# Kernel optimization log

Hardware: AMD Instinct MI355X
Metric: run time of the kernel (lower is better)

## Reference

```python
import jax, jax.numpy as jnp
import numpy as np

B, T, C = 2, 2048, 1280
H, D = 10, 128  # n_head, head_dim (n_kv_head == n_head, so no repeat)
EPS = 1e-5
NEG = -1e9


def setup_inputs() -> dict:
    key = jax.random.key(0)
    ks = jax.random.split(key, 7)
    s = 0.02
    return {
        "x": jax.random.normal(ks[0], (B, T, C), jnp.float32),
        "cos": jax.random.normal(ks[1], (1, 1, T, D // 2), jnp.float32),
        "sin": jax.random.normal(ks[2], (1, 1, T, D // 2), jnp.float32),
        "Wq": jax.random.normal(ks[3], (C, C), jnp.float32) * s,
        "Wk": jax.random.normal(ks[4], (C, C), jnp.float32) * s,
        "Wv": jax.random.normal(ks[5], (C, C), jnp.float32) * s,
        "Wproj": jax.random.normal(ks[6], (C, C), jnp.float32) * s,
    }


def _rope(x, cos, sin):
    # x: [b,h,t,d]; split last dim in half
    x1, x2 = jnp.split(x, 2, axis=-1)
    y1 = x1 * cos + x2 * sin
    y2 = -x1 * sin + x2 * cos
    return jnp.concatenate([y1, y2], axis=-1)


def _rms_norm(x):
    mean = jnp.mean(x * x, axis=-1, keepdims=True)
    return x / jnp.sqrt(mean + EPS)


def reference(x, cos, sin, Wq, Wk, Wv, Wproj):
    b, t, c = x.shape
    # nn.Linear: y = x @ W.T; weights stored [out, in]
    q = (x @ Wq.T).reshape(b, t, H, D).transpose(0, 2, 1, 3)  # [b,h,t,d]
    k = (x @ Wk.T).reshape(b, t, H, D).transpose(0, 2, 1, 3)
    v = (x @ Wv.T).reshape(b, t, H, D).transpose(0, 2, 1, 3)
    q = _rms_norm(_rope(q, cos, sin))
    k = _rms_norm(_rope(k, cos, sin))
    scale = 1.0 / jnp.sqrt(jnp.float32(D))
    scores = jnp.einsum("bhqd,bhkd->bhqk", q, k) * scale
    mask = jnp.triu(jnp.ones((t, t), scores.dtype), k=1)  # 1 above diagonal
    scores = scores + mask * NEG
    attn = jax.nn.softmax(scores, axis=-1)
    y = jnp.einsum("bhqk,bhkd->bhqd", attn, v)
    y = y.transpose(0, 2, 1, 3).reshape(b, t, c)
    return y @ Wproj.T
```

## Files before the change

kernel.cpp:

```cpp
#include <hip/hip_runtime.h>
#include <hip/hip_bf16.h>

#define B_ 2
#define T_ 2048
#define C_ 1280
#define H_ 10
#define D_ 128
#define BT_ (B_*T_)

typedef __hip_bfloat16 bf16;
typedef __attribute__((ext_vector_type(8))) short short8;
typedef __attribute__((ext_vector_type(4))) float f32x4;

__device__ __forceinline__ float bf2f(bf16 v){ return __bfloat162float(v); }
__device__ __forceinline__ bf16  f2bf(float v){ return __float2bfloat16(v); }
__device__ __forceinline__ void stv(bf16* p, float v){ *p = f2bf(v); }
__device__ __forceinline__ void stv(float* p, float v){ *p = v; }

struct alignas(8) bf4 { bf16 a,b,c,d; };

__device__ __forceinline__ void gl2lds(const bf16* g, bf16* l) {
    __builtin_amdgcn_global_load_lds(
        (const __attribute__((address_space(1))) void*)g,
        (__attribute__((address_space(3))) void*)l,
        16, 0, 0);
}

__global__ __launch_bounds__(256)
void cvt(const float* __restrict__ s, bf16* __restrict__ d)
{
    const int i = (blockIdx.x*256 + threadIdx.x)*4;
    const float4 v = *(const float4*)(s + i);
    bf4 o = { f2bf(v.x), f2bf(v.y), f2bf(v.z), f2bf(v.w) };
    *(bf4*)(d + i) = o;
}

__global__ __launch_bounds__(256)
void cvtW(const float* __restrict__ s0, const float* __restrict__ s1,
          const float* __restrict__ s2, const float* __restrict__ s3,
          bf16* __restrict__ d)
{
    const int w = blockIdx.y;
    const float* s = (w==0)?s0:(w==1)?s1:(w==2)?s2:s3;
    const int i = (blockIdx.x*256 + threadIdx.x)*4;
    const float4 v = *(const float4*)(s + i);
    bf4 o = { f2bf(v.x), f2bf(v.y), f2bf(v.z), f2bf(v.w) };
    *(bf4*)(d + (size_t)w*C_*C_ + i) = o;
}

template <typename OT>
__global__ __launch_bounds__(256,3)
void gemm_nt(const bf16* __restrict__ A, const bf16* __restrict__ Wb,
             OT* __restrict__ O0, OT* __restrict__ O1, OT* __restrict__ O2)
{
    __shared__ __align__(16) bf16 As[128*64];
    __shared__ __align__(16) bf16 Bs[128*64];
    const int z = blockIdx.z;
    const bf16* Wm = Wb + (size_t)z*C_*C_;
    OT*         Om = (z==0) ? O0 : (z==1) ? O1 : O2;
    const int wave = threadIdx.x >> 6;
    const int lane = threadIdx.x & 63;
    const int l15 = lane & 15, quad = lane >> 4;
    const int row0 = blockIdx.x*128;
    const int col0 = blockIdx.y*128;
    const int wm = (wave>>1)*64, wn = (wave&1)*64;
    const int srow = lane >> 3;
    const int scol = (lane & 7)*8;

    const f32x4 fzero = {0.f,0.f,0.f,0.f};
    f32x4 acc[4][4];
    #pragma unroll
    for (int i=0;i<4;i++)
        #pragma unroll
        for (int j=0;j<4;j++) acc[i][j] = fzero;

    const bf16* Ag = A  + (size_t)(row0 + wave*32 + srow)*C_ + scol;
    const bf16* Bg = Wm + (size_t)(col0 + wave*32 + srow)*C_ + scol;
    bf16* Al = As + (wave*32)*64;
    bf16* Bl = Bs + (wave*32)*64;

    for (int k0 = 0; k0 < C_; k0 += 64) {
        __syncthreads();
        #pragma unroll
        for (int i=0;i<4;i++){
            gl2lds(Ag + (size_t)i*8*C_ + k0, Al + i*8*64);
            gl2lds(Bg + (size_t)i*8*C_ + k0, Bl + i*8*64);
        }
        asm volatile("s_waitcnt vmcnt(0)" ::: "memory");
        __syncthreads();
        #pragma unroll
        for (int h=0; h<2; ++h) {
            short8 af[4], bfv[4];
            #pragma unroll
            for (int mt=0; mt<4; ++mt) af[mt]  = *(const short8*)(As + (wm + mt*16 + l15)*64 + h*32 + quad*8);
            #pragma unroll
            for (int nt=0; nt<4; ++nt) bfv[nt] = *(const short8*)(Bs + (wn + nt*16 + l15)*64 + h*32 + quad*8);
            #pragma unroll
            for (int mt=0; mt<4; ++mt)
                #pragma unroll
                for (int nt=0; nt<4; ++nt)
                    acc[mt][nt] = __builtin_amdgcn_mfma_f32_16x16x32_bf16(af[mt], bfv[nt], acc[mt][nt], 0,0,0);
        }
    }
    #pragma unroll
    for (int mt=0; mt<4; ++mt)
        #pragma unroll
        for (int nt=0; nt<4; ++nt)
            #pragma unroll
            for (int r=0; r<4; ++r)
                stv(&Om[(size_t)(row0 + wm + mt*16 + quad*4 + r)*C_ + col0 + wn + nt*16 + l15], acc[mt][nt][r]);
}

__global__ __launch_bounds__(256)
void rope_rms(bf16* __restrict__ q, bf16* __restrict__ k,
              const float* __restrict__ cosp, const float* __restrict__ sinp)
{
    const int wave = threadIdx.x >> 6, lane = threadIdx.x & 63;
    const long rb = (long)blockIdx.x*4 + wave;
    const int h = (int)(rb % H_);
    const long bt = rb / H_;
    const int t = (int)(bt % T_);
    bf16* buf = blockIdx.y ? k : q;
    const size_t base = (size_t)bt*C_ + (size_t)h*D_;
    float x1 = bf2f(buf[base + lane]);
    float x2 = bf2f(buf[base + 64 + lane]);
    float c  = cosp[(size_t)t*64 + lane];
    float s  = sinp[(size_t)t*64 + lane];
    float y1 =  x1*c + x2*s;
    float y2 = -x1*s + x2*c;
    float ss = y1*y1 + y2*y2;
    #pragma unroll
    for (int off=1; off<64; off<<=1) ss += __shfl_xor(ss, off);
    float sc = rsqrtf(ss*(1.0f/128.0f) + 1e-5f);
    buf[base + lane]      = f2bf(y1*sc);
    buf[base + 64 + lane] = f2bf(y2*sc);
}

__global__ __launch_bounds__(256)
void vtrans(const bf16* __restrict__ V, bf16* __restrict__ Vt)
{
    __shared__ float st[64][65];
    const int tid = threadIdx.x;
    const int bh = blockIdx.z;
    const int b = bh / H_, h = bh % H_;
    const int t0 = blockIdx.x*64, d0 = blockIdx.y*64;
    #pragma unroll
    for (int i=0;i<16;i++){
        int e = tid + i*256;
        int r = e >> 6, dd = e & 63;
        st[r][dd] = bf2f(V[(size_t)(b*T_ + t0 + r)*C_ + h*D_ + d0 + dd]);
    }
    __syncthreads();
    #pragma unroll
    for (int i=0;i<16;i++){
        int e = tid + i*256;
        int dd = e >> 6, r = e & 63;
        Vt[((size_t)bh*D_ + d0 + dd)*T_ + t0 + r] = f2bf(st[r][dd]);
    }
}

#define M0_ 11.3137085f
__global__ __launch_bounds__(256,3)
void attn(const bf16* __restrict__ Q, const bf16* __restrict__ K,
          const bf16* __restrict__ Vt, bf16* __restrict__ Y,
          bf16* __restrict__ opart, float* __restrict__ lpart)
{
    __shared__ __align__(16) bf16 kbuf[64*128];
    __shared__ __align__(16) bf16 vbuf[128*64];
    __shared__ __align__(16) bf16 ptile[4][16*72];
    const int wave = threadIdx.x >> 6, lane = threadIdx.x & 63;
    const int l15 = lane & 15, quad = lane >> 4;
    const int bid = blockIdx.x;
    const int bh = bid/48, u = bid%48;
    const bool split = (u < 32);
    const int t  = split ? (31 - (u>>1)) : (47 - u);
    const int s  = split ? (u & 1) : 0;
    const int b = bh / H_, h = bh % H_;
    const int t0 = t*64;
    const int nch = t + 1;
    const int cbeg = split ? (s*nch)>>1 : 0;
    const int cend = split ? ((s+1)*nch)>>1 : nch;
    const size_t base = (size_t)b*T_*C_ + (size_t)h*D_;
    const bf16* Kbh = K + base;
    const bf16* Vbh = Vt + (size_t)bh*D_*T_;
    const int t0w = t0 + wave*16;
    const float scale = 0.08838834764831845f;
    bf16* pt = ptile[wave];

    short8 qa[4];
    {
        const bf16* qp = Q + base + (size_t)(t0w + l15)*C_ + quad*8;
        #pragma unroll
        for (int kb4=0; kb4<4; ++kb4) qa[kb4] = *(const short8*)(qp + kb4*32);
    }
    const f32x4 fzero = {0.f,0.f,0.f,0.f};
    f32x4 o[8];
    #pragma unroll
    for (int dt=0; dt<8; ++dt) o[dt] = fzero;
    float lp[4] = {0.f,0.f,0.f,0.f};

    const int vr_off = lane >> 3;
    const int vu     = lane & 7;

    for (int ch=cbeg; ch<cend; ++ch) {
        const int k0 = ch*64;
        __syncthreads();
        #pragma unroll
        for (int j=0;j<4;j++){
            const int row = wave*16 + j*4 + quad;
            const int ug  = (l15 - row) & 15;
            gl2lds(Kbh + (size_t)(k0 + row)*C_ + ug*8, &kbuf[(wave*16 + j*4)*128]);
        }
        #pragma unroll
        for (int j=0;j<4;j++){
            const int r  = wave*32 + j*8 + vr_off;
            const int ug = (vu - r) & 7;
            gl2lds(Vbh + (size_t)r*T_ + k0 + ug*8, &vbuf[(wave*32 + j*8)*64]);
        }
        asm volatile("s_waitcnt vmcnt(0)" ::: "memory");
        __syncthreads();

        f32x4 sc4[4];
        #pragma unroll
        for (int c=0;c<4;c++) sc4[c] = fzero;
        #pragma unroll
        for (int c=0;c<4;c++){
            short8 kf[4];
            #pragma unroll
            for (int kb4=0; kb4<4; ++kb4) {
                const int up = (kb4*4 + quad + l15) & 15;
                kf[kb4] = *(const short8*)(&kbuf[(c*16 + l15)*128 + up*8]);
            }
            #pragma unroll
            for (int kb4=0; kb4<4; ++kb4)
                sc4[c] = __builtin_amdgcn_mfma_f32_16x16x32_bf16(qa[kb4], kf[kb4], sc4[c], 0,0,0);
        }
        const bool lastc = (ch == nch-1);
        #pragma unroll
        for (int r=0; r<4; ++r) {
            const int rt = t0w + quad*4 + r;
            float v[4];
            #pragma unroll
            for (int c=0;c<4;c++) v[c] = sc4[c][r]*scale;
            if (lastc) {
                #pragma unroll
                for (int c=0;c<4;c++) if (k0 + c*16 + l15 > rt) v[c] = -1e30f;
            }
            float p[4];
            #pragma unroll
            for (int c=0;c<4;c++) p[c] = __expf(v[c] - M0_);
            lp[r] += (p[0]+p[1]) + (p[2]+p[3]);
            #pragma unroll
            for (int c=0;c<4;c++) pt[(quad*4+r)*72 + c*16 + l15] = f2bf(p[c]);
        }
        asm volatile("s_waitcnt lgkmcnt(0)" ::: "memory");
        short8 pa[2];
        #pragma unroll
        for (int ks=0; ks<2; ++ks)
            pa[ks] = *(const short8*)(pt + l15*72 + ks*32 + quad*8);
        #pragma unroll
        for (int dt=0; dt<8; ++dt) {
            #pragma unroll
            for (int ks=0; ks<2; ++ks) {
                const int up = (ks*4 + quad + l15) & 7;
                short8 vF = *(const short8*)(&vbuf[(dt*16 + l15)*64 + up*8]);
                o[dt] = __builtin_amdgcn_mfma_f32_16x16x32_bf16(pa[ks], vF, o[dt], 0,0,0);
            }
        }
    }

    #pragma unroll
    for (int r=0; r<4; ++r) {
        #pragma unroll
        for (int off=1; off<16; off<<=1) lp[r] += __shfl_xor(lp[r], off);
    }
    if (!split) {
        float li[4];
        #pragma unroll
        for (int r=0; r<4; ++r) li[r] = 1.0f/lp[r];
        #pragma unroll
        for (int dt=0; dt<8; ++dt)
            #pragma unroll
            for (int r=0; r<4; ++r)
                Y[base + (size_t)(t0w + quad*4 + r)*C_ + dt*16 + l15] = f2bf(o[dt][r]*li[r]);
    } else {
        const int slot = ((bh*16 + (t-16))<<1) | s;
        bf16* ob = opart + (size_t)slot*8192 + (wave*16)*128;
        #pragma unroll
        for (int dt=0; dt<8; ++dt)
            #pragma unroll
            for (int r=0; r<4; ++r)
                ob[(quad*4+r)*128 + dt*16 + l15] = f2bf(o[dt][r]);
        if (l15 == 0) {
            #pragma unroll
            for (int r=0; r<4; ++r) lpart[(size_t)slot*64 + wave*16 + quad*4 + r] = lp[r];
        }
    }
}

__global__ __launch_bounds__(256)
void combine2(const bf16* __restrict__ opart, const float* __restrict__ lpart,
              bf16* __restrict__ Y)
{
    const int tt = blockIdx.x;
    const int bh = tt >> 4;
    const int t = 16 + (tt & 15);
    const int b = bh / H_, h = bh % H_;
    const int row = threadIdx.x >> 2;
    const int dseg = (threadIdx.x & 3)*32;
    const float li = 1.0f/(lpart[(size_t)(2*tt)*64 + row] + lpart[(size_t)(2*tt+1)*64 + row]);
    const bf16* p0 = opart + (size_t)(2*tt)*8192   + row*128 + dseg;
    const bf16* p1 = opart + (size_t)(2*tt+1)*8192 + row*128 + dseg;
    bf16 ov[32];
    #pragma unroll
    for (int e=0;e<32;e++) ov[e] = f2bf((bf2f(p0[e]) + bf2f(p1[e]))*li);
    bf16* yp = Y + (size_t)b*T_*C_ + (size_t)(t*64+row)*C_ + (size_t)h*D_ + dseg;
    #pragma unroll
    for (int v=0; v<4; ++v) *(short8*)(yp + v*8) = *(const short8*)(&ov[v*8]);
}

extern "C" void kernel_launch(void* const* d_in, const int* in_sizes, int n_in,
                              void* d_out, int out_size, void* d_ws, size_t ws_size,
                              hipStream_t stream)
{
    const float* x    = (const float*)d_in[0];
    const float* cosp = (const float*)d_in[1];
    const float* sinp = (const float*)d_in[2];
    const float* Wq   = (const float*)d_in[3];
    const float* Wk   = (const float*)d_in[4];
    const float* Wv   = (const float*)d_in[5];
    const float* Wp   = (const float*)d_in[6];
    float* out = (float*)d_out;

    const size_t NE = (size_t)BT_ * C_;
    const size_t NW = (size_t)C_ * C_;
    bf16* xb = (bf16*)d_ws;
    bf16* wb = xb + NE;
    bf16* q  = wb + 4*NW;
    bf16* k  = q + NE;
    bf16* v  = k + NE;
    bf16* y  = v + NE;
    bf16* vT = y + NE;
    bf16* op = vT + NE;
    float* lpart = (float*)(op + (size_t)640*8192);

    cvt<<<dim3(NE/1024), 256, 0, stream>>>(x, xb);
    cvtW<<<dim3(NW/1024, 4), 256, 0, stream>>>(Wq, Wk, Wv, Wp, wb);
    gemm_nt<bf16><<<dim3(BT_/128, C_/128, 3), 256, 0, stream>>>(xb, wb, q, k, v);
    rope_rms<<<dim3(BT_*H_/4, 2), 256, 0, stream>>>(q, k, cosp, sinp);
    vtrans<<<dim3(T_/64, D_/64, B_*H_), 256, 0, stream>>>(v, vT);
    attn<<<dim3(B_*H_*48), 256, 0, stream>>>(q, k, vT, y, op, lpart);
    combine2<<<dim3(320), 256, 0, stream>>>(op, lpart, y);
    gemm_nt<float><<<dim3(BT_/128, C_/128, 1), 256, 0, stream>>>(y, wb + 3*NW, out, out, out);
}
```

Measured before the change: 260.7 us.

## Enlarge attention query tile to 128 rows so each K/V chunk is reused twice

Each attention block now processes 128 query rows (32 per wave, as two 16-row groups) instead of 64. Every K/V chunk loaded into LDS therefore feeds twice as many MFMAs, halving K/V global traffic and barrier count per query row. The block ordering changes to heavy-first with the head index as the fastest-varying dimension, and the split/combine bookkeeping is resized to match. In exchange the kernel uses more registers per wave and launches fewer blocks, and causal masking now applies to the last two chunks.

Result: slower. 302.3 us (+16.0%).

```diff
diff --git a/kernel.cpp b/kernel.cpp
--- a/kernel.cpp
+++ b/kernel.cpp
@@ -167,37 +167,40 @@
 {
     __shared__ __align__(16) bf16 kbuf[64*128];
     __shared__ __align__(16) bf16 vbuf[128*64];
-    __shared__ __align__(16) bf16 ptile[4][16*72];
+    __shared__ __align__(16) bf16 ptile[4][32*72];
     const int wave = threadIdx.x >> 6, lane = threadIdx.x & 63;
     const int l15 = lane & 15, quad = lane >> 4;
     const int bid = blockIdx.x;
-    const int bh = bid/48, u = bid%48;
-    const bool split = (u < 32);
-    const int t  = split ? (31 - (u>>1)) : (47 - u);
+    const int u = bid/20, bh = bid%20;
+    const bool split = (u < 24);
+    const int tp = split ? (15 - (u>>1)) : (27 - u);
     const int s  = split ? (u & 1) : 0;
     const int b = bh / H_, h = bh % H_;
-    const int t0 = t*64;
-    const int nch = t + 1;
-    const int cbeg = split ? (s*nch)>>1 : 0;
-    const int cend = split ? ((s+1)*nch)>>1 : nch;
+    const int t0 = tp*128;
+    const int nch = 2*tp + 2;
+    const int cbeg = split ? s*(tp+1) : 0;
+    const int cend = split ? (s+1)*(tp+1) : nch;
     const size_t base = (size_t)b*T_*C_ + (size_t)h*D_;
     const bf16* Kbh = K + base;
     const bf16* Vbh = Vt + (size_t)bh*D_*T_;
-    const int t0w = t0 + wave*16;
+    const int t0w = t0 + wave*32;
     const float scale = 0.08838834764831845f;
     bf16* pt = ptile[wave];
 
-    short8 qa[4];
-    {
-        const bf16* qp = Q + base + (size_t)(t0w + l15)*C_ + quad*8;
-        #pragma unroll
-        for (int kb4=0; kb4<4; ++kb4) qa[kb4] = *(const short8*)(qp + kb4*32);
+    short8 qa[2][4];
+    #pragma unroll
+    for (int rg=0; rg<2; ++rg) {
+        const bf16* qp = Q + base + (size_t)(t0w + rg*16 + l15)*C_ + quad*8;
+        #pragma unroll
+        for (int kb4=0; kb4<4; ++kb4) qa[rg][kb4] = *(const short8*)(qp + kb4*32);
     }
     const f32x4 fzero = {0.f,0.f,0.f,0.f};
-    f32x4 o[8];
-    #pragma unroll
-    for (int dt=0; dt<8; ++dt) o[dt] = fzero;
-    float lp[4] = {0.f,0.f,0.f,0.f};
+    f32x4 o[2][8];
+    #pragma unroll
+    for (int rg=0; rg<2; ++rg)
+        #pragma unroll
+        for (int dt=0; dt<8; ++dt) o[rg][dt] = fzero;
+    float lp[2][4] = {{0.f,0.f,0.f,0.f},{0.f,0.f,0.f,0.f}};
 
     const int vr_off = lane >> 3;
     const int vu     = lane & 7;
@@ -220,9 +223,11 @@
         asm volatile("s_waitcnt vmcnt(0)" ::: "memory");
         __syncthreads();
 
-        f32x4 sc4[4];
-        #pragma unroll
-        for (int c=0;c<4;c++) sc4[c] = fzero;
+        f32x4 sc4[2][4];
+        #pragma unroll
+        for (int rg=0; rg<2; ++rg)
+            #pragma unroll
+            for (int c=0;c<4;c++) sc4[rg][c] = fzero;
         #pragma unroll
         for (int c=0;c<4;c++){
             short8 kf[4];
@@ -232,68 +237,87 @@
                 kf[kb4] = *(const short8*)(&kbuf[(c*16 + l15)*128 + up*8]);
             }
             #pragma unroll
-            for (int kb4=0; kb4<4; ++kb4)
-                sc4[c] = __builtin_amdgcn_mfma_f32_16x16x32_bf16(qa[kb4], kf[kb4], sc4[c], 0,0,0);
-        }
-        const bool lastc = (ch == nch-1);
-        #pragma unroll
-        for (int r=0; r<4; ++r) {
-            const int rt = t0w + quad*4 + r;
-            float v[4];
-            #pragma unroll
-            for (int c=0;c<4;c++) v[c] = sc4[c][r]*scale;
-            if (lastc) {
-                #pragma unroll
-                for (int c=0;c<4;c++) if (k0 + c*16 + l15 > rt) v[c] = -1e30f;
+            for (int kb4=0; kb4<4; ++kb4) {
+                sc4[0][c] = __builtin_amdgcn_mfma_f32_16x16x32_bf16(qa[0][kb4], kf[kb4], sc4[0][c], 0,0,0);
+                sc4[1][c] = __builtin_amdgcn_mfma_f32_16x16x32_bf16(qa[1][kb4], kf[kb4], sc4[1][c], 0,0,0);
             }
-            float p[4];
-            #pragma unroll
-            for (int c=0;c<4;c++) p[c] = __expf(v[c] - M0_);
-            lp[r] += (p[0]+p[1]) + (p[2]+p[3]);
-            #pragma unroll
-            for (int c=0;c<4;c++) pt[(quad*4+r)*72 + c*16 + l15] = f2bf(p[c]);
+        }
+        const bool maskc = (ch >= nch-2);
+        #pragma unroll
+        for (int rg=0; rg<2; ++rg) {
+            #pragma unroll
+            for (int r=0; r<4; ++r) {
+                const int rt = t0w + rg*16 + quad*4 + r;
+                float v[4];
+                #pragma unroll
+                for (int c=0;c<4;c++) v[c] = sc4[rg][c][r]*scale;
+                if (maskc) {
+                    #pragma unroll
+                    for (int c=0;c<4;c++) if (k0 + c*16 + l15 > rt) v[c] = -1e30f;
+                }
+                float p[4];
+                #pragma unroll
+                for (int c=0;c<4;c++) p[c] = __expf(v[c] - M0_);
+                lp[rg][r] += (p[0]+p[1]) + (p[2]+p[3]);
+                #pragma unroll
+                for (int c=0;c<4;c++) pt[(rg*16 + quad*4 + r)*72 + c*16 + l15] = f2bf(p[c]);
+            }
         }
         asm volatile("s_waitcnt lgkmcnt(0)" ::: "memory");
-        short8 pa[2];
-        #pragma unroll
-        for (int ks=0; ks<2; ++ks)
-            pa[ks] = *(const short8*)(pt + l15*72 + ks*32 + quad*8);
+        short8 pa[2][2];
+        #pragma unroll
+        for (int rg=0; rg<2; ++rg)
+            #pragma unroll
+            for (int ks=0; ks<2; ++ks)
+                pa[rg][ks] = *(const short8*)(pt + (rg*16 + l15)*72 + ks*32 + quad*8);
         #pragma unroll
         for (int dt=0; dt<8; ++dt) {
             #pragma unroll
             for (int ks=0; ks<2; ++ks) {
                 const int up = (ks*4 + quad + l15) & 7;
                 short8 vF = *(const short8*)(&vbuf[(dt*16 + l15)*64 + up*8]);
-                o[dt] = __builtin_amdgcn_mfma_f32_16x16x32_bf16(pa[ks], vF, o[dt], 0,0,0);
+                o[0][dt] = __builtin_amdgcn_mfma_f32_16x16x32_bf16(pa[0][ks], vF, o[0][dt], 0,0,0);
+                o[1][dt] = __builtin_amdgcn_mfma_f32_16x16x32_bf16(pa[1][ks], vF, o[1][dt], 0,0,0);
             }
         }
     }
 
     #pragma unroll
-    for (int r=0; r<4; ++r) {
-        #pragma unroll
-        for (int off=1; off<16; off<<=1) lp[r] += __shfl_xor(lp[r], off);
-    }
+    for (int rg=0; rg<2; ++rg)
+        #pragma unroll
+        for (int r=0; r<4; ++r) {
+            #pragma unroll
+            for (int off=1; off<16; off<<=1) lp[rg][r] += __shfl_xor(lp[rg][r], off);
+        }
     if (!split) {
-        float li[4];
-        #pragma unroll
-        for (int r=0; r<4; ++r) li[r] = 1.0f/lp[r];
-        #pragma unroll
-        for (int dt=0; dt<8; ++dt)
-            #pragma unroll
-            for (int r=0; r<4; ++r)
-                Y[base + (size_t)(t0w + quad*4 + r)*C_ + dt*16 + l15] = f2bf(o[dt][r]*li[r]);
+        float li[2][4];
+        #pragma unroll
+        for (int rg=0; rg<2; ++rg)
+            #pragma unroll
+            for (int r=0; r<4; ++r) li[rg][r] = 1.0f/lp[rg][r];
+        #pragma unroll
+        for (int rg=0; rg<2; ++rg)
+            #pragma unroll
+            for (int dt=0; dt<8; ++dt)
+                #pragma unroll
+                for (int r=0; r<4; ++r)
+                    Y[base + (size_t)(t0w + rg*16 + quad*4 + r)*C_ + dt*16 + l15] = f2bf(o[rg][dt][r]*li[rg][r]);
     } else {
-        const int slot = ((bh*16 + (t-16))<<1) | s;
-        bf16* ob = opart + (size_t)slot*8192 + (wave*16)*128;
-        #pragma unroll
-        for (int dt=0; dt<8; ++dt)
-            #pragma unroll
-            for (int r=0; r<4; ++r)
-                ob[(quad*4+r)*128 + dt*16 + l15] = f2bf(o[dt][r]);
+        const int slot = ((bh*12 + (tp-4))<<1) | s;
+        bf16* ob = opart + (size_t)slot*16384;
+        #pragma unroll
+        for (int rg=0; rg<2; ++rg)
+            #pragma unroll
+            for (int dt=0; dt<8; ++dt)
+                #pragma unroll
+                for (int r=0; r<4; ++r)
+                    ob[(size_t)(wave*32 + rg*16 + quad*4 + r)*128 + dt*16 + l15] = f2bf(o[rg][dt][r]);
         if (l15 == 0) {
             #pragma unroll
-            for (int r=0; r<4; ++r) lpart[(size_t)slot*64 + wave*16 + quad*4 + r] = lp[r];
+            for (int rg=0; rg<2; ++rg)
+                #pragma unroll
+                for (int r=0; r<4; ++r)
+                    lpart[(size_t)slot*128 + wave*32 + rg*16 + quad*4 + r] = lp[rg][r];
         }
     }
 }
@@ -303,20 +327,20 @@
               bf16* __restrict__ Y)
 {
     const int tt = blockIdx.x;
-    const int bh = tt >> 4;
-    const int t = 16 + (tt & 15);
+    const int bh = tt / 12;
+    const int tp = 4 + (tt % 12);
     const int b = bh / H_, h = bh % H_;
-    const int row = threadIdx.x >> 2;
-    const int dseg = (threadIdx.x & 3)*32;
-    const float li = 1.0f/(lpart[(size_t)(2*tt)*64 + row] + lpart[(size_t)(2*tt+1)*64 + row]);
-    const bf16* p0 = opart + (size_t)(2*tt)*8192   + row*128 + dseg;
-    const bf16* p1 = opart + (size_t)(2*tt+1)*8192 + row*128 + dseg;
-    bf16 ov[32];
-    #pragma unroll
-    for (int e=0;e<32;e++) ov[e] = f2bf((bf2f(p0[e]) + bf2f(p1[e]))*li);
-    bf16* yp = Y + (size_t)b*T_*C_ + (size_t)(t*64+row)*C_ + (size_t)h*D_ + dseg;
-    #pragma unroll
-    for (int v=0; v<4; ++v) *(short8*)(yp + v*8) = *(const short8*)(&ov[v*8]);
+    const int row = threadIdx.x >> 1;
+    const int d0 = (threadIdx.x & 1)*64;
+    const float li = 1.0f/(lpart[(size_t)(2*tt)*128 + row] + lpart[(size_t)(2*tt+1)*128 + row]);
+    const bf16* p0 = opart + (size_t)(2*tt)*16384   + row*128 + d0;
+    const bf16* p1 = opart + (size_t)(2*tt+1)*16384 + row*128 + d0;
+    bf16 ov[64];
+    #pragma unroll
+    for (int e=0;e<64;e++) ov[e] = f2bf((bf2f(p0[e]) + bf2f(p1[e]))*li);
+    bf16* yp = Y + (size_t)b*T_*C_ + (size_t)(tp*128+row)*C_ + (size_t)h*D_ + d0;
+    #pragma unroll
+    for (int v=0; v<8; ++v) *(short8*)(yp + v*8) = *(const short8*)(&ov[v*8]);
 }
 
 extern "C" void kernel_launch(void* const* d_in, const int* in_sizes, int n_in,
@@ -342,14 +366,14 @@
     bf16* y  = v + NE;
     bf16* vT = y + NE;
     bf16* op = vT + NE;
-    float* lpart = (float*)(op + (size_t)640*8192);
+    float* lpart = (float*)(op + (size_t)480*16384);
 
     cvt<<<dim3(NE/1024), 256, 0, stream>>>(x, xb);
     cvtW<<<dim3(NW/1024, 4), 256, 0, stream>>>(Wq, Wk, Wv, Wp, wb);
     gemm_nt<bf16><<<dim3(BT_/128, C_/128, 3), 256, 0, stream>>>(xb, wb, q, k, v);
     rope_rms<<<dim3(BT_*H_/4, 2), 256, 0, stream>>>(q, k, cosp, sinp);
     vtrans<<<dim3(T_/64, D_/64, B_*H_), 256, 0, stream>>>(v, vT);
-    attn<<<dim3(B_*H_*48), 256, 0, stream>>>(q, k, vT, y, op, lpart);
-    combine2<<<dim3(320), 256, 0, stream>>>(op, lpart, y);
+    attn<<<dim3(560), 256, 0, stream>>>(q, k, vT, y, op, lpart);
+    combine2<<<dim3(240), 256, 0, stream>>>(op, lpart, y);
     gemm_nt<float><<<dim3(BT_/128, C_/128, 1), 256, 0, stream>>>(y, wb + 3*NW, out, out, out);
 }
```

## Split attention KV range into fixed 8-chunk segments for balanced blocks

Applied to the files above, without the earlier changes.

Replaces the two-way split of the upper query tiles with fixed segments of at most 8 KV chunks each, so every attention block does roughly equal work. The grid grows from 960 to 1600 blocks, ordered heaviest-first and interleaved across heads. A generalized combine kernel sums up to four partial outputs and denominators per query tile. This is meant to reduce tail imbalance across CUs, at the cost of more partial-output traffic, a larger combine step, and bf16 rounding of more partials.

Result: faster. 248.8 us (-4.6%).

```diff
diff --git a/kernel.cpp b/kernel.cpp
--- a/kernel.cpp
+++ b/kernel.cpp
@@ -170,16 +170,19 @@
     __shared__ __align__(16) bf16 ptile[4][16*72];
     const int wave = threadIdx.x >> 6, lane = threadIdx.x & 63;
     const int l15 = lane & 15, quad = lane >> 4;
-    const int bid = blockIdx.x;
-    const int bh = bid/48, u = bid%48;
-    const bool split = (u < 32);
-    const int t  = split ? (31 - (u>>1)) : (47 - u);
-    const int s  = split ? (u & 1) : 0;
+    const int bh = blockIdx.x % 20;
+    const int u  = blockIdx.x / 20;
+    int m, seg;
+    if (u < 32)      { m = 31 - (u>>2); seg = u & 3; }
+    else if (u < 56) { const int v2 = u-32; m = 23 - v2/3; seg = v2%3; }
+    else if (u < 72) { const int v2 = u-56; m = 15 - (v2>>1); seg = v2&1; }
+    else             { m = 7 - (u-72); seg = 0; }
     const int b = bh / H_, h = bh % H_;
-    const int t0 = t*64;
-    const int nch = t + 1;
-    const int cbeg = split ? (s*nch)>>1 : 0;
-    const int cend = split ? ((s+1)*nch)>>1 : nch;
+    const int t0 = m*64;
+    const int nch = m + 1;
+    const int cbeg = seg*8;
+    const int cend = min(cbeg+8, nch);
+    const bool direct = (m < 8);
     const size_t base = (size_t)b*T_*C_ + (size_t)h*D_;
     const bf16* Kbh = K + base;
     const bf16* Vbh = Vt + (size_t)bh*D_*T_;
@@ -274,7 +277,7 @@
         #pragma unroll
         for (int off=1; off<16; off<<=1) lp[r] += __shfl_xor(lp[r], off);
     }
-    if (!split) {
+    if (direct) {
         float li[4];
         #pragma unroll
         for (int r=0; r<4; ++r) li[r] = 1.0f/lp[r];
@@ -284,7 +287,8 @@
             for (int r=0; r<4; ++r)
                 Y[base + (size_t)(t0w + quad*4 + r)*C_ + dt*16 + l15] = f2bf(o[dt][r]*li[r]);
     } else {
-        const int slot = ((bh*16 + (t-16))<<1) | s;
+        const int off = (m<16) ? (m-8)*2 : (m<24) ? 16 + (m-16)*3 : 40 + (m-24)*4;
+        const int slot = bh*72 + off + seg;
         bf16* ob = opart + (size_t)slot*8192 + (wave*16)*128;
         #pragma unroll
         for (int dt=0; dt<8; ++dt)
@@ -299,22 +303,33 @@
 }
 
 __global__ __launch_bounds__(256)
-void combine2(const bf16* __restrict__ opart, const float* __restrict__ lpart,
+void combineN(const bf16* __restrict__ opart, const float* __restrict__ lpart,
               bf16* __restrict__ Y)
 {
     const int tt = blockIdx.x;
-    const int bh = tt >> 4;
-    const int t = 16 + (tt & 15);
+    const int bh = tt / 24;
+    const int m  = 8 + (tt % 24);
+    const int nseg = (m + 8) >> 3;
+    const int off = (m<16) ? (m-8)*2 : (m<24) ? 16 + (m-16)*3 : 40 + (m-24)*4;
+    const int slot0 = bh*72 + off;
     const int b = bh / H_, h = bh % H_;
     const int row = threadIdx.x >> 2;
-    const int dseg = (threadIdx.x & 3)*32;
-    const float li = 1.0f/(lpart[(size_t)(2*tt)*64 + row] + lpart[(size_t)(2*tt+1)*64 + row]);
-    const bf16* p0 = opart + (size_t)(2*tt)*8192   + row*128 + dseg;
-    const bf16* p1 = opart + (size_t)(2*tt+1)*8192 + row*128 + dseg;
+    const int d0 = (threadIdx.x & 3)*32;
+    float l = 0.f;
+    for (int s=0; s<nseg; ++s) l += lpart[(size_t)(slot0+s)*64 + row];
+    const float li = 1.0f/l;
+    float acc[32];
+    #pragma unroll
+    for (int e=0;e<32;e++) acc[e] = 0.f;
+    for (int s=0; s<nseg; ++s) {
+        const bf16* p = opart + (size_t)(slot0+s)*8192 + row*128 + d0;
+        #pragma unroll
+        for (int e=0;e<32;e++) acc[e] += bf2f(p[e]);
+    }
     bf16 ov[32];
     #pragma unroll
-    for (int e=0;e<32;e++) ov[e] = f2bf((bf2f(p0[e]) + bf2f(p1[e]))*li);
-    bf16* yp = Y + (size_t)b*T_*C_ + (size_t)(t*64+row)*C_ + (size_t)h*D_ + dseg;
+    for (int e=0;e<32;e++) ov[e] = f2bf(acc[e]*li);
+    bf16* yp = Y + (size_t)b*T_*C_ + (size_t)(m*64+row)*C_ + (size_t)h*D_ + d0;
     #pragma unroll
     for (int v=0; v<4; ++v) *(short8*)(yp + v*8) = *(const short8*)(&ov[v*8]);
 }
@@ -342,14 +357,14 @@
     bf16* y  = v + NE;
     bf16* vT = y + NE;
     bf16* op = vT + NE;
-    float* lpart = (float*)(op + (size_t)640*8192);
+    float* lpart = (float*)(op + (size_t)1440*8192);
 
     cvt<<<dim3(NE/1024), 256, 0, stream>>>(x, xb);
     cvtW<<<dim3(NW/1024, 4), 256, 0, stream>>>(Wq, Wk, Wv, Wp, wb);
     gemm_nt<bf16><<<dim3(BT_/128, C_/128, 3), 256, 0, stream>>>(xb, wb, q, k, v);
     rope_rms<<<dim3(BT_*H_/4, 2), 256, 0, stream>>>(q, k, cosp, sinp);
     vtrans<<<dim3(T_/64, D_/64, B_*H_), 256, 0, stream>>>(v, vT);
-    attn<<<dim3(B_*H_*48), 256, 0, stream>>>(q, k, vT, y, op, lpart);
-    combine2<<<dim3(320), 256, 0, stream>>>(op, lpart, y);
+    attn<<<dim3(1600), 256, 0, stream>>>(q, k, vT, y, op, lpart);
+    combineN<<<dim3(480), 256, 0, stream>>>(op, lpart, y);
     gemm_nt<float><<<dim3(BT_/128, C_/128, 1), 256, 0, stream>>>(y, wb + 3*NW, out, out, out);
 }
```
